# Performance work log

Measured on AMD Instinct MI355X. Metric: run time of the kernel, lower is better.

The kernel has to match this reference:

```python
import jax, jax.numpy as jnp
import numpy as np

D_MODEL = 2048
N_HEADS = 16
D_K = D_MODEL // N_HEADS
BATCH = 2
SEQ = 2048


def _rope(q, k):
    # q,k: [B, H, S, Dk], interleaved even/odd RoPE as in the torch source
    seq_len = q.shape[2]
    d = q.shape[-1]
    freqs = 1.0 / (10000.0 ** (jnp.arange(0, d, 2.0, dtype=jnp.float32) / d))  # [Dk/2]
    pos = jnp.arange(seq_len, dtype=jnp.float32)
    ang = pos[:, None] * freqs[None, :]          # [S, Dk/2]
    sin, cos = jnp.sin(ang), jnp.cos(ang)

    def rot(t):
        te, to = t[..., ::2], t[..., 1::2]
        out = jnp.stack([te * cos - to * sin, te * sin + to * cos], axis=-1)
        return out.reshape(t.shape)

    return rot(q), rot(k)


def setup_inputs() -> dict:
    key = jax.random.key(0)
    ks = jax.random.split(key, 5)
    scale = 1.0 / np.sqrt(D_MODEL)
    return {
        "x": jax.random.normal(ks[0], (BATCH, SEQ, D_MODEL), jnp.float32),
        "w_q": jax.random.normal(ks[1], (D_MODEL, D_MODEL), jnp.float32) * scale,
        "w_k": jax.random.normal(ks[2], (D_MODEL, D_MODEL), jnp.float32) * scale,
        "w_v": jax.random.normal(ks[3], (D_MODEL, D_MODEL), jnp.float32) * scale,
        "w_o": jax.random.normal(ks[4], (D_MODEL, D_MODEL), jnp.float32) * scale,
        "b_o": jnp.zeros((D_MODEL,), jnp.float32),
    }


def reference(x, w_q, w_k, w_v, w_o, b_o):
    B, S, D = x.shape
    H, Dk = N_HEADS, D_K
    # nn.Linear: y = x @ W.T
    q = (x @ w_q.T).reshape(B, S, H, Dk).transpose(0, 2, 1, 3)
    k = (x @ w_k.T).reshape(B, S, H, Dk).transpose(0, 2, 1, 3)
    v = (x @ w_v.T).reshape(B, S, H, Dk).transpose(0, 2, 1, 3)
    q, k = _rope(q, k)
    scores = jnp.einsum('bhqd,bhkd->bhqk', q, k) / jnp.sqrt(jnp.float32(Dk))
    causal = jnp.tril(jnp.ones((S, S), bool))  # True = keep
    scores = jnp.where(causal[None, None], scores, -jnp.inf)
    attn = jax.nn.softmax(scores, axis=-1)
    out = jnp.einsum('bhqk,bhkd->bhqd', attn, v)
    out = out.transpose(0, 2, 1, 3).reshape(B, S, D)
    return out @ w_o.T + b_o
```

## Files before the change

### kernel.cpp

```cpp
#include <hip/hip_runtime.h>

#define D_MODEL 2048
#define NHEADS  16
#define DK      128
#define BATCH   2
#define SEQ     2048
#define MTOT    (BATCH*SEQ)

typedef unsigned short u16;
typedef unsigned int   u32;
typedef __bf16 bf16x8 __attribute__((ext_vector_type(8)));
typedef float  f32x4  __attribute__((ext_vector_type(4)));

__device__ __forceinline__ float b2f(u16 u) {
  return __uint_as_float(((u32)u) << 16);
}
__device__ __forceinline__ u16 f2b(float f) {
  u32 x = __float_as_uint(f);
  x += 0x7fffu + ((x >> 16) & 1u);
  return (u16)(x >> 16);
}

__device__ __forceinline__ void gl2lds16(const u16* g, u16* l) {
  __builtin_amdgcn_global_load_lds(
      (const __attribute__((address_space(1))) void*)g,
      (__attribute__((address_space(3))) void*)l, 16, 0, 0);
}

__global__ __launch_bounds__(256) void cvt_k(const float* __restrict__ in,
                                             u16* __restrict__ out, int n4) {
  int i = blockIdx.x * 256 + threadIdx.x;
  if (i >= n4) return;
  float4 v = ((const float4*)in)[i];
  u32 lo = (u32)f2b(v.x) | ((u32)f2b(v.y) << 16);
  u32 hi = (u32)f2b(v.z) | ((u32)f2b(v.w) << 16);
  ((uint2*)out)[i] = make_uint2(lo, hi);
}

__global__ __launch_bounds__(256) void cvt4_k(const float* __restrict__ a, const float* __restrict__ b,
                                              const float* __restrict__ c, const float* __restrict__ d,
                                              u16* __restrict__ oa, u16* __restrict__ ob,
                                              u16* __restrict__ oc, u16* __restrict__ od, int n4) {
  int z = blockIdx.y;
  const float* in = (z == 0) ? a : (z == 1) ? b : (z == 2) ? c : d;
  u16* out = (z == 0) ? oa : (z == 1) ? ob : (z == 2) ? oc : od;
  int i = blockIdx.x * 256 + threadIdx.x;
  if (i >= n4) return;
  float4 v = ((const float4*)in)[i];
  u32 lo = (u32)f2b(v.x) | ((u32)f2b(v.y) << 16);
  u32 hi = (u32)f2b(v.z) | ((u32)f2b(v.w) << 16);
  ((uint2*)out)[i] = make_uint2(lo, hi);
}

__global__ __launch_bounds__(256) void gemm_bt(const u16* __restrict__ A,
                                               const u16* __restrict__ B,
                                               const int M, const int N, const int K,
                                               u16* __restrict__ outb,
                                               float* __restrict__ outf,
                                               const float* __restrict__ bias,
                                               const int mode) {
  __shared__ __align__(16) u16 As[16 * 512];
  __shared__ __align__(16) u16 Bs[16 * 512];

  const int t    = threadIdx.x;
  const int lane = t & 63;
  const int wave = t >> 6;
  const int wm   = wave >> 1, wn = wave & 1;
  const int quad = lane >> 4, l16 = lane & 15;
  const int m0 = blockIdx.y * 128, n0 = blockIdx.x * 128;
  const int sr = lane & 15, sc = lane >> 4;

  const u16* ap[4]; u16* ad[4];
  const u16* bp[4]; u16* bd[4];
#pragma unroll
  for (int j = 0; j < 4; ++j) {
    int id = wave * 4 + j;
    int kc = id >> 3, mt = id & 7;
    ap[j] = A + (size_t)(m0 + mt * 16 + sr) * K + kc * 32 + sc * 8;
    ad[j] = As + id * 512;
    bp[j] = B + (size_t)(n0 + mt * 16 + sr) * K + kc * 32 + sc * 8;
    bd[j] = Bs + id * 512;
  }

  f32x4 acc[4][4] = {};

  for (int k0 = 0; k0 < K; k0 += 64) {
    __syncthreads();
    gl2lds16(ap[0] + k0, ad[0]);
    gl2lds16(ap[1] + k0, ad[1]);
    gl2lds16(ap[2] + k0, ad[2]);
    gl2lds16(ap[3] + k0, ad[3]);
    gl2lds16(bp[0] + k0, bd[0]);
    gl2lds16(bp[1] + k0, bd[1]);
    gl2lds16(bp[2] + k0, bd[2]);
    gl2lds16(bp[3] + k0, bd[3]);
    __syncthreads();

#pragma unroll
    for (int kc = 0; kc < 2; ++kc) {
      bf16x8 af[4], bfr[4];
#pragma unroll
      for (int i = 0; i < 4; ++i)
        af[i] = *(const bf16x8*)&As[(kc * 8 + wm * 4 + i) * 512 + lane * 8];
#pragma unroll
      for (int j = 0; j < 4; ++j)
        bfr[j] = *(const bf16x8*)&Bs[(kc * 8 + wn * 4 + j) * 512 + lane * 8];
#pragma unroll
      for (int i = 0; i < 4; ++i)
#pragma unroll
        for (int j = 0; j < 4; ++j)
          acc[i][j] = __builtin_amdgcn_mfma_f32_16x16x32_bf16(af[i], bfr[j], acc[i][j], 0, 0, 0);
    }
  }

  if (mode == 0) {
#pragma unroll
    for (int i = 0; i < 4; ++i)
#pragma unroll
      for (int j = 0; j < 4; ++j)
#pragma unroll
        for (int rr = 0; rr < 4; ++rr) {
          int row = m0 + wm * 64 + i * 16 + quad * 4 + rr;
          int col = n0 + wn * 64 + j * 16 + l16;
          outf[(size_t)row * N + col] = acc[i][j][rr] + bias[col];
        }
  } else {
    const int tens = n0 >> 11;
    const int h    = (n0 & 2047) >> 7;
    const bool doRope = (tens < 2);
    const float mult = (tens == 0) ? 0.08838834764831845f : 1.0f;
#pragma unroll
    for (int j = 0; j < 4; ++j) {
      const int d = wn * 64 + j * 16 + l16;
      const float freq = exp2f(-0.20762050593045951f * (float)(d >> 1));
      const float sgn  = (d & 1) ? 1.f : -1.f;
#pragma unroll
      for (int i = 0; i < 4; ++i)
#pragma unroll
        for (int rr = 0; rr < 4; ++rr) {
          int row = m0 + wm * 64 + i * 16 + quad * 4 + rr;
          int b = row >> 11;
          int s = row & (SEQ - 1);
          float v = acc[i][j][rr];
          if (doRope) {
            float sn, cs;
            __sincosf((float)s * freq, &sn, &cs);
            float pv = __shfl_xor(v, 1);
            v = (v * cs + sgn * pv * sn) * mult;
          }
          outb[(size_t)tens * 8388608 + (((size_t)(b * NHEADS + h)) * SEQ + s) * DK + d] = f2b(v);
        }
    }
  }
}

__global__ __launch_bounds__(256) void vt_k(const u16* __restrict__ V,
                                            u16* __restrict__ Vt) {
  constexpr int LDT = 72;
  __shared__ __align__(16) u16 tile[64 * LDT];
  const int s0 = blockIdx.x * 64, d0 = blockIdx.y * 64, bh = blockIdx.z;
  const u16* in = V + (size_t)bh * SEQ * DK;
  u16* out = Vt + (size_t)bh * DK * SEQ;
  const int t = threadIdx.x;
  const int r = t >> 3, cg = t & 7;
#pragma unroll
  for (int half = 0; half < 2; ++half) {
    uint4 v = *(const uint4*)(in + (size_t)(s0 + r + half * 32) * DK + d0 + cg * 8);
    *(uint4*)&tile[(r + half * 32) * LDT + cg * 8] = v;
  }
  __syncthreads();
#pragma unroll
  for (int half = 0; half < 2; ++half) {
    int d = (t >> 3) + half * 32;
    __align__(16) u16 tmp[8];
#pragma unroll
    for (int i = 0; i < 8; ++i) tmp[i] = tile[(cg * 8 + i) * LDT + d];
    *(uint4*)(out + (size_t)(d0 + d) * SEQ + s0 + cg * 8) = *(const uint4*)tmp;
  }
}

__global__ __launch_bounds__(256, 4) void attn_k(const u16* __restrict__ Q,
                                                 const u16* __restrict__ K,
                                                 const u16* __restrict__ Vt,
                                                 u16* __restrict__ out) {
  __shared__ __align__(16) u16 smem[8192 + 8192 + 4096];
  u16* Ks = smem;
  u16* Vs = smem + 8192;

  const int t    = threadIdx.x;
  const int lane = t & 63;
  const int wave = t >> 6;
  const int quad = lane >> 4, l16 = lane & 15;
  u16* Psw = smem + 16384 + wave * 1024;
  const int pmask = (l16 & 7) << 3;
  const int qt = (int)gridDim.x - 1 - (int)blockIdx.x;
  const int bh = blockIdx.y;
  const size_t baseQK = (size_t)bh * SEQ * DK;
  const size_t baseV  = (size_t)bh * DK * SEQ;
  const int qw = qt * 64 + wave * 16;
  const int qglob = qw + l16;

  bf16x8 qf[4];
#pragma unroll
  for (int kc = 0; kc < 4; ++kc)
    qf[kc] = *(const bf16x8*)(Q + baseQK + (size_t)(qw + l16) * DK + kc * 32 + quad * 8);

  f32x4 oacc[8] = {};
  float m_run = -1e30f, l_run = 0.f;

  const int sr = lane & 15, sc = lane >> 4;
  const u16* kp[4]; u16* kd[4];
  const u16* vp[4]; u16* vd[4];
#pragma unroll
  for (int j = 0; j < 4; ++j) {
    int lin = wave * 4 + j;
    int knt = lin >> 2, kkc = lin & 3;
    kp[j] = K + baseQK + (size_t)(knt * 16 + sr) * DK + kkc * 32 + sc * 8;
    kd[j] = Ks + lin * 512;
    int vkc = lin >> 3, vnt = lin & 7;
    vp[j] = Vt + baseV + (size_t)(vnt * 16 + sr) * SEQ + vkc * 32 + sc * 8;
    vd[j] = Vs + lin * 512;
  }

  const int kend = (qt + 1) * 64;
  for (int k0 = 0; k0 < kend; k0 += 64) {
    __syncthreads();
#pragma unroll
    for (int j = 0; j < 4; ++j) gl2lds16(kp[j], kd[j]);
#pragma unroll
    for (int j = 0; j < 4; ++j) gl2lds16(vp[j], vd[j]);
#pragma unroll
    for (int j = 0; j < 4; ++j) { kp[j] += (size_t)64 * DK; vp[j] += 64; }
    __syncthreads();

    if (k0 >= qw + 16) continue;

    f32x4 s[4] = {};
#pragma unroll
    for (int kc = 0; kc < 4; ++kc) {
#pragma unroll
      for (int nt = 0; nt < 4; ++nt) {
        bf16x8 kf = *(const bf16x8*)&Ks[(nt * 4 + kc) * 512 + lane * 8];
        s[nt] = __builtin_amdgcn_mfma_f32_16x16x32_bf16(kf, qf[kc], s[nt], 0, 0, 0);
      }
    }

    float p[4][4];
    float newm = m_run;
    if (k0 + 63 > qw) {
#pragma unroll
      for (int nt = 0; nt < 4; ++nt)
#pragma unroll
        for (int r = 0; r < 4; ++r) {
          int key = k0 + nt * 16 + quad * 4 + r;
          float v = (key <= qglob) ? s[nt][r] : -1e30f;
          p[nt][r] = v;
          newm = fmaxf(newm, v);
        }
    } else {
#pragma unroll
      for (int nt = 0; nt < 4; ++nt)
#pragma unroll
        for (int r = 0; r < 4; ++r) {
          p[nt][r] = s[nt][r];
          newm = fmaxf(newm, s[nt][r]);
        }
    }
    newm = fmaxf(newm, __shfl_xor(newm, 16));
    newm = fmaxf(newm, __shfl_xor(newm, 32));
    float lsum = 0.f;
#pragma unroll
    for (int nt = 0; nt < 4; ++nt)
#pragma unroll
      for (int r = 0; r < 4; ++r) {
        float e = __expf(p[nt][r] - newm);
        p[nt][r] = e;
        lsum += e;
      }
    lsum += __shfl_xor(lsum, 16);
    lsum += __shfl_xor(lsum, 32);
    float alpha = __expf(m_run - newm);
    l_run = l_run * alpha + lsum;
    m_run = newm;

#pragma unroll
    for (int nt = 0; nt < 4; ++nt) {
      u32 lo = (u32)f2b(p[nt][0]) | ((u32)f2b(p[nt][1]) << 16);
      u32 hi = (u32)f2b(p[nt][2]) | ((u32)f2b(p[nt][3]) << 16);
      *(uint2*)&Psw[l16 * 64 + ((nt * 16 + quad * 4) ^ pmask)] = make_uint2(lo, hi);
    }

#pragma unroll
    for (int r = 0; r < 4; ++r) {
      float av = __shfl(alpha, quad * 4 + r);
#pragma unroll
      for (int nt = 0; nt < 8; ++nt) oacc[nt][r] *= av;
    }

#pragma unroll
    for (int kcp = 0; kcp < 2; ++kcp) {
      bf16x8 pf = *(const bf16x8*)&Psw[l16 * 64 + ((kcp * 32 + quad * 8) ^ pmask)];
#pragma unroll
      for (int nt = 0; nt < 8; ++nt) {
        bf16x8 vf = *(const bf16x8*)&Vs[(kcp * 8 + nt) * 512 + lane * 8];
        oacc[nt] = __builtin_amdgcn_mfma_f32_16x16x32_bf16(pf, vf, oacc[nt], 0, 0, 0);
      }
    }
  }

  constexpr int LDO = 136;
  float invl = 1.f / l_run;
  __syncthreads();
#pragma unroll
  for (int r = 0; r < 4; ++r) {
    float iv = __shfl(invl, quad * 4 + r);
#pragma unroll
    for (int nt = 0; nt < 8; ++nt)
      smem[(wave * 16 + quad * 4 + r) * LDO + nt * 16 + l16] = f2b(oacc[nt][r] * iv);
  }
  __syncthreads();
  const int b = bh >> 4, h = bh & 15;
#pragma unroll
  for (int pss = 0; pss < 4; ++pss) {
    int row = (t >> 4) + pss * 16;
    uint4 v = *(const uint4*)&smem[row * LDO + (t & 15) * 8];
    *(uint4*)(out + ((size_t)(b * SEQ + qt * 64 + row)) * D_MODEL + h * DK + (t & 15) * 8) = v;
  }
}

extern "C" void kernel_launch(void* const* d_in, const int* in_sizes, int n_in,
                              void* d_out, int out_size, void* d_ws, size_t ws_size,
                              hipStream_t stream) {
  const float* x  = (const float*)d_in[0];
  const float* wq = (const float*)d_in[1];
  const float* wk = (const float*)d_in[2];
  const float* wv = (const float*)d_in[3];
  const float* wo = (const float*)d_in[4];
  const float* bo = (const float*)d_in[5];
  float* out = (float*)d_out;

  char* wsb = (char*)d_ws;
  u16* xb    = (u16*)(wsb + 0);
  u16* wqb   = (u16*)(wsb + 16777216);
  u16* wkb   = (u16*)(wsb + 25165824);
  u16* wvb   = (u16*)(wsb + 33554432);
  u16* wob   = (u16*)(wsb + 41943040);
  u16* Qb    = (u16*)(wsb + 50331648);
  u16* Kb    = (u16*)(wsb + 67108864);
  u16* Vb    = (u16*)(wsb + 83886080);
  u16* attnb = xb;
  u16* Vtb   = wqb;

  cvt_k<<<8192, 256, 0, stream>>>(x, xb, MTOT * D_MODEL / 4);
  cvt4_k<<<dim3(4096, 4), 256, 0, stream>>>(wq, wk, wv, wo, wqb, wkb, wvb, wob,
                                            D_MODEL * D_MODEL / 4);

  gemm_bt<<<dim3(48, 32), 256, 0, stream>>>(xb, wqb, MTOT, 3 * D_MODEL, D_MODEL,
                                            Qb, nullptr, nullptr, 1);

  vt_k<<<dim3(SEQ / 64, DK / 64, BATCH * NHEADS), 256, 0, stream>>>(Vb, Vtb);

  attn_k<<<dim3(SEQ / 64, BATCH * NHEADS), 256, 0, stream>>>(Qb, Kb, Vtb, attnb);

  gemm_bt<<<dim3(16, 32), 256, 0, stream>>>(attnb, wob, MTOT, D_MODEL, D_MODEL,
                                            nullptr, out, bo, 0);
}
```

Baseline: 548.2 us.

## Triple-buffer GEMM with 256x128 tiles, 8 waves, and async LDS prefetch

Replaces the single-buffered 128x128 GEMM with a 256x128-tile, 512-thread kernel. Global-to-LDS loads go into a three-stage ring buffer issued two tiles ahead, with vmcnt waits and raw barriers so loads overlap MFMA work. It also raises wave priority around the MFMA block. The cost is more LDS (about 144KB per block at two blocks per CU) and fewer blocks, which can hurt occupancy and tail balance.

```diff
diff --git a/kernel.cpp b/kernel.cpp
--- a/kernel.cpp
+++ b/kernel.cpp
@@ -52,65 +52,90 @@
   ((uint2*)out)[i] = make_uint2(lo, hi);
 }
 
-__global__ __launch_bounds__(256) void gemm_bt(const u16* __restrict__ A,
-                                               const u16* __restrict__ B,
-                                               const int M, const int N, const int K,
-                                               u16* __restrict__ outb,
-                                               float* __restrict__ outf,
-                                               const float* __restrict__ bias,
-                                               const int mode) {
-  __shared__ __align__(16) u16 As[16 * 512];
-  __shared__ __align__(16) u16 Bs[16 * 512];
+__global__ __launch_bounds__(512, 2) void gemm256(const u16* __restrict__ A,
+                                                  const u16* __restrict__ B,
+                                                  const int M, const int N, const int K,
+                                                  u16* __restrict__ outb,
+                                                  float* __restrict__ outf,
+                                                  const float* __restrict__ bias,
+                                                  const int mode) {
+  __shared__ __align__(16) u16 smem[3 * 24576];
 
   const int t    = threadIdx.x;
   const int lane = t & 63;
   const int wave = t >> 6;
   const int wm   = wave >> 1, wn = wave & 1;
   const int quad = lane >> 4, l16 = lane & 15;
-  const int m0 = blockIdx.y * 128, n0 = blockIdx.x * 128;
+  const int m0 = blockIdx.y * 256, n0 = blockIdx.x * 128;
   const int sr = lane & 15, sc = lane >> 4;
 
-  const u16* ap[4]; u16* ad[4];
-  const u16* bp[4]; u16* bd[4];
-#pragma unroll
-  for (int j = 0; j < 4; ++j) {
-    int id = wave * 4 + j;
-    int kc = id >> 3, mt = id & 7;
-    ap[j] = A + (size_t)(m0 + mt * 16 + sr) * K + kc * 32 + sc * 8;
-    ad[j] = As + id * 512;
-    bp[j] = B + (size_t)(n0 + mt * 16 + sr) * K + kc * 32 + sc * 8;
-    bd[j] = Bs + id * 512;
+  const u16* agp[4]; u16* ald[4];
+  const u16* bgp[2]; u16* bld[2];
+#pragma unroll
+  for (int q = 0; q < 4; ++q) {
+    int a = wave * 4 + q;
+    int kc = a >> 4, mt = a & 15;
+    agp[q] = A + (size_t)(m0 + mt * 16 + sr) * K + kc * 32 + sc * 8;
+    ald[q] = smem + a * 512;
+  }
+#pragma unroll
+  for (int q = 0; q < 2; ++q) {
+    int b = wave * 2 + q;
+    int kc = b >> 3, nt = b & 7;
+    bgp[q] = B + (size_t)(n0 + nt * 16 + sr) * K + kc * 32 + sc * 8;
+    bld[q] = smem + 16384 + b * 512;
   }
 
   f32x4 acc[4][4] = {};
-
-  for (int k0 = 0; k0 < K; k0 += 64) {
-    __syncthreads();
-    gl2lds16(ap[0] + k0, ad[0]);
-    gl2lds16(ap[1] + k0, ad[1]);
-    gl2lds16(ap[2] + k0, ad[2]);
-    gl2lds16(ap[3] + k0, ad[3]);
-    gl2lds16(bp[0] + k0, bd[0]);
-    gl2lds16(bp[1] + k0, bd[1]);
-    gl2lds16(bp[2] + k0, bd[2]);
-    gl2lds16(bp[3] + k0, bd[3]);
-    __syncthreads();
-
+  const int NT = K >> 6;
+
+#pragma unroll
+  for (int q = 0; q < 4; ++q) { gl2lds16(agp[q], ald[q]);         agp[q] += 64; }
+#pragma unroll
+  for (int q = 0; q < 2; ++q) { gl2lds16(bgp[q], bld[q]);         bgp[q] += 64; }
+#pragma unroll
+  for (int q = 0; q < 4; ++q) { gl2lds16(agp[q], ald[q] + 24576); agp[q] += 64; }
+#pragma unroll
+  for (int q = 0; q < 2; ++q) { gl2lds16(bgp[q], bld[q] + 24576); bgp[q] += 64; }
+
+  int cur = 0;
+  for (int tt = 0; tt < NT; ++tt) {
+    if (tt + 1 < NT) asm volatile("s_waitcnt vmcnt(6)" ::: "memory");
+    else             asm volatile("s_waitcnt vmcnt(0)" ::: "memory");
+    __builtin_amdgcn_s_barrier();
+    asm volatile("" ::: "memory");
+
+    if (tt + 2 < NT) {
+      int nb = cur + 2; if (nb >= 3) nb -= 3;
+      const int off = nb * 24576;
+#pragma unroll
+      for (int q = 0; q < 4; ++q) { gl2lds16(agp[q], ald[q] + off); agp[q] += 64; }
+#pragma unroll
+      for (int q = 0; q < 2; ++q) { gl2lds16(bgp[q], bld[q] + off); bgp[q] += 64; }
+    }
+
+    const u16* As = smem + cur * 24576;
+    const u16* Bs = As + 16384;
 #pragma unroll
     for (int kc = 0; kc < 2; ++kc) {
-      bf16x8 af[4], bfr[4];
+      bf16x8 af[4], bfv[4];
 #pragma unroll
       for (int i = 0; i < 4; ++i)
-        af[i] = *(const bf16x8*)&As[(kc * 8 + wm * 4 + i) * 512 + lane * 8];
+        af[i] = *(const bf16x8*)&As[(kc * 16 + wm * 4 + i) * 512 + lane * 8];
 #pragma unroll
       for (int j = 0; j < 4; ++j)
-        bfr[j] = *(const bf16x8*)&Bs[(kc * 8 + wn * 4 + j) * 512 + lane * 8];
+        bfv[j] = *(const bf16x8*)&Bs[(kc * 8 + wn * 4 + j) * 512 + lane * 8];
+      __builtin_amdgcn_s_setprio(1);
 #pragma unroll
       for (int i = 0; i < 4; ++i)
 #pragma unroll
         for (int j = 0; j < 4; ++j)
-          acc[i][j] = __builtin_amdgcn_mfma_f32_16x16x32_bf16(af[i], bfr[j], acc[i][j], 0, 0, 0);
-    }
+          acc[i][j] = __builtin_amdgcn_mfma_f32_16x16x32_bf16(af[i], bfv[j], acc[i][j], 0, 0, 0);
+      __builtin_amdgcn_s_setprio(0);
+    }
+    asm volatile("" ::: "memory");
+    __builtin_amdgcn_s_barrier();
+    cur = cur + 1; if (cur >= 3) cur -= 3;
   }
 
   if (mode == 0) {
@@ -355,13 +380,13 @@
   cvt4_k<<<dim3(4096, 4), 256, 0, stream>>>(wq, wk, wv, wo, wqb, wkb, wvb, wob,
                                             D_MODEL * D_MODEL / 4);
 
-  gemm_bt<<<dim3(48, 32), 256, 0, stream>>>(xb, wqb, MTOT, 3 * D_MODEL, D_MODEL,
+  gemm256<<<dim3(48, 16), 512, 0, stream>>>(xb, wqb, MTOT, 3 * D_MODEL, D_MODEL,
                                             Qb, nullptr, nullptr, 1);
 
   vt_k<<<dim3(SEQ / 64, DK / 64, BATCH * NHEADS), 256, 0, stream>>>(Vb, Vtb);
 
   attn_k<<<dim3(SEQ / 64, BATCH * NHEADS), 256, 0, stream>>>(Qb, Kb, Vtb, attnb);
 
-  gemm_bt<<<dim3(16, 32), 256, 0, stream>>>(attnb, wob, MTOT, D_MODEL, D_MODEL,
+  gemm256<<<dim3(16, 16), 512, 0, stream>>>(attnb, wob, MTOT, D_MODEL, D_MODEL,
                                             nullptr, out, bo, 0);
 }
```

New measurement: 492.4 us. 1.11x faster.
